# Performance work log

Hardware: AMD Instinct MI355X
Metric: run time of the kernel (lower is better)

## Reference

```python
import jax, jax.numpy as jnp
import numpy as np

HEADS = 16
HEAD_DIM = 64  # embed_size // heads = 1024 // 16


def setup_inputs() -> dict:
    key = jax.random.key(0)
    ks = jax.random.split(key, 9)
    N, Sq, E, C = 4, 2048, 1024, 512
    Skv = 2 * Sq  # keys/values seq must equal doubled query seq (see view trick)
    return {
        "values": jax.random.normal(ks[0], (N, Skv, E), dtype=jnp.float32),
        "keys": jax.random.normal(ks[1], (N, Skv, E), dtype=jnp.float32),
        "queries": jax.random.normal(ks[2], (N, Sq, E), dtype=jnp.float32),
        "mask": jax.random.randint(ks[3], (N, Skv, HEADS, HEADS), 0, 2, dtype=jnp.int32),
        "condition": jax.random.normal(ks[4], (N, Sq, C), dtype=jnp.float32),
        "Wc": jax.random.normal(ks[5], (E, C), dtype=jnp.float32) * 0.02,
        "bc": jax.random.normal(ks[6], (E,), dtype=jnp.float32) * 0.02,
        "Wo": jax.random.normal(ks[7], (E, E), dtype=jnp.float32) * 0.02,
        "bo": jax.random.normal(ks[8], (E,), dtype=jnp.float32) * 0.02,
    }


def reference(values, keys, queries, mask, condition, Wc, bc, Wo, bo):
    N = queries.shape[0]
    H, D = HEADS, HEAD_DIM
    # condition_linear + concat: (N, Sq, 2E) -> view doubles seq -> (N, 2Sq, H, D)
    cond_feat = jnp.einsum('nsc,ec->nse', condition, Wc) + bc
    cq = jnp.concatenate([queries, cond_feat], axis=-1).reshape(N, -1, H, D)
    k = keys.reshape(N, -1, H, D)    # (N, 2Sq, H, D)
    v = values.reshape(N, -1, H, D)  # (N, 2Sq, H, D)
    # per-(batch,seq) heads-by-heads attention, exactly as the torch matmul does
    att = jnp.einsum('nshd,nsed->nshe', cq, k) / jnp.sqrt(jnp.float32(D))
    att = jnp.where(mask == 0, jnp.float32(-1e20), att)
    att = jax.nn.softmax(att, axis=-1)
    out = jnp.einsum('nshe,nsed->nshd', att, v).reshape(N, -1, H * D)
    return jnp.einsum('nsk,ek->nse', out, Wo) + bo
```

## Files before the change

### kernel.cpp

```cpp
#include <hip/hip_runtime.h>
#include <hip/hip_bf16.h>
#include <type_traits>

#define NB   4
#define SQ   2048
#define SKV  4096
#define EMB  1024
#define CDIM 512

typedef __attribute__((ext_vector_type(8))) short short8;
typedef __attribute__((ext_vector_type(4))) float f32x4;

__device__ __forceinline__ float b2f(ushort u) {
    union { unsigned int i; float f; } v;
    v.i = ((unsigned int)u) << 16;
    return v.f;
}
__device__ __forceinline__ ushort f2b(float f) {
    union { float f; unsigned int i; } v; v.f = f;
    unsigned int x = v.i;
    return (ushort)((x + 0x7fffu + ((x >> 16) & 1u)) >> 16);
}

__device__ __forceinline__ void glds16(const ushort* gp, ushort* lp) {
    __builtin_amdgcn_global_load_lds(
        (const __attribute__((address_space(1))) unsigned int*)gp,
        (__attribute__((address_space(3))) unsigned int*)lp,
        16, 0, 0);
}

__global__ __launch_bounds__(256)
void cvt_f32_bf16(const float* __restrict__ in, ushort* __restrict__ out, int n4)
{
    const int i = blockIdx.x * 256 + threadIdx.x;
    if (i < n4) {
        float4 v = ((const float4*)in)[i];
        ushort4 o;
        o.x = f2b(v.x); o.y = f2b(v.y); o.z = f2b(v.z); o.w = f2b(v.w);
        ((ushort4*)out)[i] = o;
    }
}

template <typename OT>
__global__ __launch_bounds__(256)
void gemm_bt_bias(const ushort* __restrict__ A, const ushort* __restrict__ B,
                  const float* __restrict__ bias, OT* __restrict__ C,
                  int M, int Nn, int K)
{
    __shared__ __attribute__((aligned(16))) ushort As[128 * 32];
    __shared__ __attribute__((aligned(16))) ushort Bs[128 * 32];

    const int tid  = threadIdx.x;
    const int wave = tid >> 6;
    const int lane = tid & 63;
    const int quad = lane >> 4;
    const int l16  = lane & 15;
    const int wr   = wave >> 1;
    const int wc   = wave & 1;

    int mTile, nTile;
    {
        const int gx = gridDim.x, gy = gridDim.y;
        const int flat = blockIdx.y * gx + blockIdx.x;
        if ((gx & 7) == 0 && gy == 8) {
            const int c = flat & 7, j = flat >> 3;
            mTile = c * (gx >> 3) + (j >> 3);
            nTile = j & 7;
        } else {
            mTile = blockIdx.x; nTile = blockIdx.y;
        }
    }
    const long mBase = (long)mTile * 128;
    const long nBase = (long)nTile * 128;

    const ushort* Ablk = A + mBase * K;
    const ushort* Bblk = B + nBase * K;

    const int lr = lane >> 2;
    const int lc = (lane & 3) * 8;
    const int c0 = wave * 2, c1 = wave * 2 + 1;
    const ushort* aG0 = Ablk + (long)(c0 * 16 + lr) * K + lc;
    const ushort* aG1 = Ablk + (long)(c1 * 16 + lr) * K + lc;
    const ushort* bG0 = Bblk + (long)(c0 * 16 + lr) * K + lc;
    const ushort* bG1 = Bblk + (long)(c1 * 16 + lr) * K + lc;
    ushort* aL0 = As + c0 * 512;
    ushort* aL1 = As + c1 * 512;
    ushort* bL0 = Bs + c0 * 512;
    ushort* bL1 = Bs + c1 * 512;

    f32x4 acc[4][4];
#pragma unroll
    for (int i = 0; i < 4; ++i)
#pragma unroll
        for (int j = 0; j < 4; ++j)
            acc[i][j] = (f32x4){0.f, 0.f, 0.f, 0.f};

    for (int k0 = 0; k0 < K; k0 += 32) {
        __syncthreads();
        glds16(aG0 + k0, aL0);
        glds16(aG1 + k0, aL1);
        glds16(bG0 + k0, bL0);
        glds16(bG1 + k0, bL1);
        __syncthreads();

        short8 af[4], bfr[4];
#pragma unroll
        for (int mt = 0; mt < 4; ++mt)
            af[mt] = *(const short8*)(As + (wr * 64 + mt * 16 + l16) * 32 + quad * 8);
#pragma unroll
        for (int nt = 0; nt < 4; ++nt)
            bfr[nt] = *(const short8*)(Bs + (wc * 64 + nt * 16 + l16) * 32 + quad * 8);

#pragma unroll
        for (int mt = 0; mt < 4; ++mt)
#pragma unroll
            for (int nt = 0; nt < 4; ++nt)
                acc[mt][nt] = __builtin_amdgcn_mfma_f32_16x16x32_bf16(
                    af[mt], bfr[nt], acc[mt][nt], 0, 0, 0);
    }

#pragma unroll
    for (int mt = 0; mt < 4; ++mt) {
#pragma unroll
        for (int nt = 0; nt < 4; ++nt) {
            const long n = nBase + wc * 64 + nt * 16 + l16;
            const float bv = bias[n];
#pragma unroll
            for (int r = 0; r < 4; ++r) {
                const long m = mBase + wr * 64 + mt * 16 + quad * 4 + r;
                if constexpr (std::is_same<OT, float>::value)
                    C[m * Nn + n] = acc[mt][nt][r] + bv;
                else
                    C[m * Nn + n] = f2b(acc[mt][nt][r] + bv);
            }
        }
    }
}

__global__ __launch_bounds__(256)
void attn_kernel(const float*  __restrict__ queries,
                 const ushort* __restrict__ condfeat,
                 const float*  __restrict__ keys,
                 const float*  __restrict__ values,
                 const int*    __restrict__ mask,
                 ushort* __restrict__ attout)
{
    __shared__ __attribute__((aligned(16))) float vbuf[4][1024];

    const int tid  = threadIdx.x;
    const int wave = tid >> 6;
    const int lane = tid & 63;
    const int l15  = lane & 15;
    const int quad = lane >> 4;
    const int p    = blockIdx.x * 4 + wave;
    const int n    = p >> 12;
    const int sh   = (p & 4095) >> 1;

    float* vb = vbuf[wave];
    const float* vrow = values + ((size_t)p << 10);
#pragma unroll
    for (int c = 0; c < 4; ++c)
        glds16((const ushort*)(vrow + c * 256 + lane * 4),
               (ushort*)(vb + c * 256));

    const int4 mv = *(const int4*)(mask + ((size_t)p << 8) + l15 * 16 + quad * 4);

    union SU { short8 v; ushort u[8]; uint w[4]; };

    const float* krow = keys + ((size_t)p << 10);
    SU ka, kb;
    {
        float kf[16];
        *(float4*)&kf[0]  = *(const float4*)(krow + l15 * 64 + quad * 8);
        *(float4*)&kf[4]  = *(const float4*)(krow + l15 * 64 + quad * 8 + 4);
        *(float4*)&kf[8]  = *(const float4*)(krow + l15 * 64 + 32 + quad * 8);
        *(float4*)&kf[12] = *(const float4*)(krow + l15 * 64 + 32 + quad * 8 + 4);
#pragma unroll
        for (int j = 0; j < 8; ++j) { ka.u[j] = f2b(kf[j]); kb.u[j] = f2b(kf[8 + j]); }
    }

    SU qa, qb;
    if (p & 1) {
        const ushort* crow = condfeat + (((size_t)n * SQ + sh) << 10);
        qa.v = *(const short8*)(crow + l15 * 64 + quad * 8);
        qb.v = *(const short8*)(crow + l15 * 64 + 32 + quad * 8);
    } else {
        const float* qrow = queries + (((size_t)n * SQ + sh) << 10);
        float qf[16];
        *(float4*)&qf[0]  = *(const float4*)(qrow + l15 * 64 + quad * 8);
        *(float4*)&qf[4]  = *(const float4*)(qrow + l15 * 64 + quad * 8 + 4);
        *(float4*)&qf[8]  = *(const float4*)(qrow + l15 * 64 + 32 + quad * 8);
        *(float4*)&qf[12] = *(const float4*)(qrow + l15 * 64 + 32 + quad * 8 + 4);
#pragma unroll
        for (int j = 0; j < 8; ++j) { qa.u[j] = f2b(qf[j]); qb.u[j] = f2b(qf[8 + j]); }
    }

    f32x4 sacc = (f32x4){0.f, 0.f, 0.f, 0.f};
    sacc = __builtin_amdgcn_mfma_f32_16x16x32_bf16(ka.v, qa.v, sacc, 0, 0, 0);
    sacc = __builtin_amdgcn_mfma_f32_16x16x32_bf16(kb.v, qb.v, sacc, 0, 0, 0);

    float s0 = (mv.x == 0) ? -1e20f : sacc[0] * 0.125f;
    float s1 = (mv.y == 0) ? -1e20f : sacc[1] * 0.125f;
    float s2 = (mv.z == 0) ? -1e20f : sacc[2] * 0.125f;
    float s3 = (mv.w == 0) ? -1e20f : sacc[3] * 0.125f;

    float mx = fmaxf(fmaxf(s0, s1), fmaxf(s2, s3));
    mx = fmaxf(mx, __shfl_xor(mx, 16));
    mx = fmaxf(mx, __shfl_xor(mx, 32));
    const float e0 = __expf(s0 - mx), e1 = __expf(s1 - mx);
    const float e2 = __expf(s2 - mx), e3 = __expf(s3 - mx);
    float sum = e0 + e1 + e2 + e3;
    sum += __shfl_xor(sum, 16);
    sum += __shfl_xor(sum, 32);
    const float inv = 1.f / sum;

    const uint pk01 = (uint)f2b(e0 * inv) | ((uint)f2b(e1 * inv) << 16);
    const uint pk23 = (uint)f2b(e2 * inv) | ((uint)f2b(e3 * inv) << 16);

    const int srcA = (quad * 32 + l15) & 63;
    const int srcB = (quad * 32 + 16 + l15) & 63;
    SU pf;
    {
        const uint w0 = (uint)__shfl((int)pk01, srcA);
        const uint w1 = (uint)__shfl((int)pk23, srcA);
        const uint w2 = (uint)__shfl((int)pk01, srcB);
        const uint w3 = (uint)__shfl((int)pk23, srcB);
        const bool lo = (lane < 32);
        pf.w[0] = lo ? w0 : 0u; pf.w[1] = lo ? w1 : 0u;
        pf.w[2] = lo ? w2 : 0u; pf.w[3] = lo ? w3 : 0u;
    }

    asm volatile("s_waitcnt vmcnt(0)" ::: "memory");

    ushort* orow = attout + ((size_t)p << 10);
    const int eb = (quad & 1) * 8;
#pragma unroll
    for (int sl = 0; sl < 4; ++sl) {
        const int d0 = sl * 16;
        SU vf;
#pragma unroll
        for (int j = 0; j < 8; ++j)
            vf.u[j] = f2b(vb[(eb + j) * 64 + d0 + l15]);
        f32x4 oacc = (f32x4){0.f, 0.f, 0.f, 0.f};
        oacc = __builtin_amdgcn_mfma_f32_16x16x32_bf16(vf.v, pf.v, oacc, 0, 0, 0);
        ushort4 o;
        o.x = f2b(oacc[0]); o.y = f2b(oacc[1]);
        o.z = f2b(oacc[2]); o.w = f2b(oacc[3]);
        *(ushort4*)(orow + l15 * 64 + d0 + quad * 4) = o;
    }
}

extern "C" void kernel_launch(void* const* d_in, const int* in_sizes, int n_in,
                              void* d_out, int out_size, void* d_ws, size_t ws_size,
                              hipStream_t stream)
{
    const float* values    = (const float*)d_in[0];
    const float* keys      = (const float*)d_in[1];
    const float* queries   = (const float*)d_in[2];
    const int*   mask      = (const int*)  d_in[3];
    const float* condition = (const float*)d_in[4];
    const float* Wc        = (const float*)d_in[5];
    const float* bc        = (const float*)d_in[6];
    const float* Wo        = (const float*)d_in[7];
    const float* bo        = (const float*)d_in[8];
    float* out = (float*)d_out;

    ushort* condfeat = (ushort*)d_ws;
    ushort* attout   = condfeat + (size_t)NB * SQ * EMB;
    ushort* cond_bf  = attout;
    ushort* Wc_bf    = attout + (size_t)NB * SQ * CDIM;
    ushort* Wo_bf    = condfeat;

    cvt_f32_bf16<<<(NB * SQ * CDIM / 4 + 255) / 256, 256, 0, stream>>>(
        condition, cond_bf, NB * SQ * CDIM / 4);
    cvt_f32_bf16<<<(EMB * CDIM / 4 + 255) / 256, 256, 0, stream>>>(
        Wc, Wc_bf, EMB * CDIM / 4);

    {
        dim3 grid((NB * SQ) / 128, EMB / 128);
        gemm_bt_bias<ushort><<<grid, 256, 0, stream>>>(
            cond_bf, Wc_bf, bc, condfeat, NB * SQ, EMB, CDIM);
    }

    attn_kernel<<<(NB * SKV) / 4, 256, 0, stream>>>(queries, condfeat, keys,
                                                    values, mask, attout);

    cvt_f32_bf16<<<(EMB * EMB / 4 + 255) / 256, 256, 0, stream>>>(
        Wo, Wo_bf, EMB * EMB / 4);

    {
        dim3 grid((NB * SKV) / 128, EMB / 128);
        gemm_bt_bias<float><<<grid, 256, 0, stream>>>(
            attout, Wo_bf, bo, out, NB * SKV, EMB, EMB);
    }
}
```

Measured before the change: 301.6 us.

## Stage K/V/Q through padded bf16 LDS with coalesced block-wide loads

The attention kernel now loads keys, values, queries and condfeat cooperatively across the whole block with contiguous nontemporal vector loads. It converts them to bf16 once and stores them in padded LDS tiles, replacing the strided per-lane global loads and the fp32 LDS buffer for V. Output is staged through LDS so each lane writes 16-byte contiguous stores. This aims to improve coalescing and cut conversion work in a memory-bound kernel, at the cost of a block barrier and extra LDS traffic.

```diff
diff --git a/kernel.cpp b/kernel.cpp
--- a/kernel.cpp
+++ b/kernel.cpp
@@ -7,9 +7,12 @@
 #define SKV  4096
 #define EMB  1024
 #define CDIM 512
+#define POSB 4
 
 typedef __attribute__((ext_vector_type(8))) short short8;
 typedef __attribute__((ext_vector_type(4))) float f32x4;
+typedef __attribute__((ext_vector_type(4))) uint  u32x4;
+typedef __attribute__((ext_vector_type(2))) uint  u32x2;
 
 __device__ __forceinline__ float b2f(ushort u) {
     union { unsigned int i; float f; } v;
@@ -20,6 +23,12 @@
     union { float f; unsigned int i; } v; v.f = f;
     unsigned int x = v.i;
     return (ushort)((x + 0x7fffu + ((x >> 16) & 1u)) >> 16);
+}
+__device__ __forceinline__ u32x2 cvt2(f32x4 v) {
+    u32x2 r;
+    r[0] = (uint)f2b(v[0]) | ((uint)f2b(v[1]) << 16);
+    r[1] = (uint)f2b(v[2]) | ((uint)f2b(v[3]) << 16);
+    return r;
 }
 
 __device__ __forceinline__ void glds16(const ushort* gp, ushort* lp) {
@@ -145,64 +154,78 @@
                  const int*    __restrict__ mask,
                  ushort* __restrict__ attout)
 {
-    __shared__ __attribute__((aligned(16))) float vbuf[4][1024];
+    __shared__ __attribute__((aligned(16))) ushort Kl[POSB * 1088];
+    __shared__ __attribute__((aligned(16))) ushort Vl[POSB * 1088];
+    __shared__ __attribute__((aligned(16))) ushort Ql[POSB * 1088];
 
     const int tid  = threadIdx.x;
     const int wave = tid >> 6;
     const int lane = tid & 63;
     const int l15  = lane & 15;
     const int quad = lane >> 4;
-    const int p    = blockIdx.x * 4 + wave;
-    const int n    = p >> 12;
-    const int sh   = (p & 4095) >> 1;
-
-    float* vb = vbuf[wave];
-    const float* vrow = values + ((size_t)p << 10);
-#pragma unroll
-    for (int c = 0; c < 4; ++c)
-        glds16((const ushort*)(vrow + c * 256 + lane * 4),
-               (ushort*)(vb + c * 256));
-
-    const int4 mv = *(const int4*)(mask + ((size_t)p << 8) + l15 * 16 + quad * 4);
-
-    union SU { short8 v; ushort u[8]; uint w[4]; };
-
-    const float* krow = keys + ((size_t)p << 10);
-    SU ka, kb;
-    {
-        float kf[16];
-        *(float4*)&kf[0]  = *(const float4*)(krow + l15 * 64 + quad * 8);
-        *(float4*)&kf[4]  = *(const float4*)(krow + l15 * 64 + quad * 8 + 4);
-        *(float4*)&kf[8]  = *(const float4*)(krow + l15 * 64 + 32 + quad * 8);
-        *(float4*)&kf[12] = *(const float4*)(krow + l15 * 64 + 32 + quad * 8 + 4);
-#pragma unroll
-        for (int j = 0; j < 8; ++j) { ka.u[j] = f2b(kf[j]); kb.u[j] = f2b(kf[8 + j]); }
-    }
-
-    SU qa, qb;
-    if (p & 1) {
-        const ushort* crow = condfeat + (((size_t)n * SQ + sh) << 10);
-        qa.v = *(const short8*)(crow + l15 * 64 + quad * 8);
-        qb.v = *(const short8*)(crow + l15 * 64 + 32 + quad * 8);
-    } else {
-        const float* qrow = queries + (((size_t)n * SQ + sh) << 10);
-        float qf[16];
-        *(float4*)&qf[0]  = *(const float4*)(qrow + l15 * 64 + quad * 8);
-        *(float4*)&qf[4]  = *(const float4*)(qrow + l15 * 64 + quad * 8 + 4);
-        *(float4*)&qf[8]  = *(const float4*)(qrow + l15 * 64 + 32 + quad * 8);
-        *(float4*)&qf[12] = *(const float4*)(qrow + l15 * 64 + 32 + quad * 8 + 4);
-#pragma unroll
-        for (int j = 0; j < 8; ++j) { qa.u[j] = f2b(qf[j]); qb.u[j] = f2b(qf[8 + j]); }
-    }
+    const int p0   = blockIdx.x * POSB;
+    const int n    = p0 >> 12;
+    const int sh0  = (p0 & 4095) >> 1;
+    const int p    = p0 + wave;
+
+    const f32x4* kg = (const f32x4*)(keys    + ((size_t)p0 << 10)) + tid;
+    const f32x4* vg = (const f32x4*)(values  + ((size_t)p0 << 10)) + tid;
+    const f32x4* qg = (const f32x4*)(queries + (((size_t)n * SQ + sh0) << 10)) + tid;
+    const u32x4* cg = (const u32x4*)(condfeat + (((size_t)n * SQ + sh0) << 10)) + tid;
+
+    f32x4 kv0 = __builtin_nontemporal_load(kg);
+    f32x4 kv1 = __builtin_nontemporal_load(kg + 256);
+    f32x4 kv2 = __builtin_nontemporal_load(kg + 512);
+    f32x4 kv3 = __builtin_nontemporal_load(kg + 768);
+    f32x4 vv0 = __builtin_nontemporal_load(vg);
+    f32x4 vv1 = __builtin_nontemporal_load(vg + 256);
+    f32x4 vv2 = __builtin_nontemporal_load(vg + 512);
+    f32x4 vv3 = __builtin_nontemporal_load(vg + 768);
+    f32x4 qv0 = __builtin_nontemporal_load(qg);
+    f32x4 qv1 = __builtin_nontemporal_load(qg + 256);
+    u32x4 cv  = __builtin_nontemporal_load(cg);
+    u32x4 mv  = __builtin_nontemporal_load(
+        (const u32x4*)(mask + ((size_t)p << 8)) + (l15 * 4 + quad));
+
+    const int eo = (tid >> 4) * 68 + (tid & 15) * 4;
+    *(u32x2*)(Kl + 0 * 1088 + eo) = cvt2(kv0);
+    *(u32x2*)(Kl + 1 * 1088 + eo) = cvt2(kv1);
+    *(u32x2*)(Kl + 2 * 1088 + eo) = cvt2(kv2);
+    *(u32x2*)(Kl + 3 * 1088 + eo) = cvt2(kv3);
+    *(u32x2*)(Vl + 0 * 1088 + eo) = cvt2(vv0);
+    *(u32x2*)(Vl + 1 * 1088 + eo) = cvt2(vv1);
+    *(u32x2*)(Vl + 2 * 1088 + eo) = cvt2(vv2);
+    *(u32x2*)(Vl + 3 * 1088 + eo) = cvt2(vv3);
+    *(u32x2*)(Ql + 0 * 1088 + eo) = cvt2(qv0);
+    *(u32x2*)(Ql + 2 * 1088 + eo) = cvt2(qv1);
+    {
+        const int cp = 1 + ((tid >> 7) << 1);
+        const int co = cp * 1088 + ((tid >> 3) & 15) * 68 + (tid & 7) * 8;
+        *(u32x2*)(Ql + co)     = (u32x2){cv[0], cv[1]};
+        *(u32x2*)(Ql + co + 4) = (u32x2){cv[2], cv[3]};
+    }
+    __syncthreads();
+
+    const ushort* Kw = Kl + wave * 1088;
+    const ushort* Vw = Vl + wave * 1088;
+    ushort*       Qw = Ql + wave * 1088;
+
+    union FU { short8 v; ushort u[8]; uint w[4]; u32x2 q[2]; };
+    const int fo = l15 * 68 + quad * 8;
+    FU ka, kb, qa, qb;
+    ka.q[0] = *(const u32x2*)(Kw + fo);      ka.q[1] = *(const u32x2*)(Kw + fo + 4);
+    kb.q[0] = *(const u32x2*)(Kw + fo + 32); kb.q[1] = *(const u32x2*)(Kw + fo + 36);
+    qa.q[0] = *(const u32x2*)(Qw + fo);      qa.q[1] = *(const u32x2*)(Qw + fo + 4);
+    qb.q[0] = *(const u32x2*)(Qw + fo + 32); qb.q[1] = *(const u32x2*)(Qw + fo + 36);
 
     f32x4 sacc = (f32x4){0.f, 0.f, 0.f, 0.f};
     sacc = __builtin_amdgcn_mfma_f32_16x16x32_bf16(ka.v, qa.v, sacc, 0, 0, 0);
     sacc = __builtin_amdgcn_mfma_f32_16x16x32_bf16(kb.v, qb.v, sacc, 0, 0, 0);
 
-    float s0 = (mv.x == 0) ? -1e20f : sacc[0] * 0.125f;
-    float s1 = (mv.y == 0) ? -1e20f : sacc[1] * 0.125f;
-    float s2 = (mv.z == 0) ? -1e20f : sacc[2] * 0.125f;
-    float s3 = (mv.w == 0) ? -1e20f : sacc[3] * 0.125f;
+    float s0 = (mv[0] == 0u) ? -1e20f : sacc[0] * 0.125f;
+    float s1 = (mv[1] == 0u) ? -1e20f : sacc[1] * 0.125f;
+    float s2 = (mv[2] == 0u) ? -1e20f : sacc[2] * 0.125f;
+    float s3 = (mv[3] == 0u) ? -1e20f : sacc[3] * 0.125f;
 
     float mx = fmaxf(fmaxf(s0, s1), fmaxf(s2, s3));
     mx = fmaxf(mx, __shfl_xor(mx, 16));
@@ -219,7 +242,7 @@
 
     const int srcA = (quad * 32 + l15) & 63;
     const int srcB = (quad * 32 + 16 + l15) & 63;
-    SU pf;
+    FU pf;
     {
         const uint w0 = (uint)__shfl((int)pk01, srcA);
         const uint w1 = (uint)__shfl((int)pk23, srcA);
@@ -230,23 +253,32 @@
         pf.w[2] = lo ? w2 : 0u; pf.w[3] = lo ? w3 : 0u;
     }
 
-    asm volatile("s_waitcnt vmcnt(0)" ::: "memory");
-
-    ushort* orow = attout + ((size_t)p << 10);
     const int eb = (quad & 1) * 8;
 #pragma unroll
     for (int sl = 0; sl < 4; ++sl) {
         const int d0 = sl * 16;
-        SU vf;
+        FU vf;
 #pragma unroll
         for (int j = 0; j < 8; ++j)
-            vf.u[j] = f2b(vb[(eb + j) * 64 + d0 + l15]);
+            vf.u[j] = Vw[(eb + j) * 68 + d0 + l15];
         f32x4 oacc = (f32x4){0.f, 0.f, 0.f, 0.f};
         oacc = __builtin_amdgcn_mfma_f32_16x16x32_bf16(vf.v, pf.v, oacc, 0, 0, 0);
-        ushort4 o;
-        o.x = f2b(oacc[0]); o.y = f2b(oacc[1]);
-        o.z = f2b(oacc[2]); o.w = f2b(oacc[3]);
-        *(ushort4*)(orow + l15 * 64 + d0 + quad * 4) = o;
+        u32x2 ow;
+        ow[0] = (uint)f2b(oacc[0]) | ((uint)f2b(oacc[1]) << 16);
+        ow[1] = (uint)f2b(oacc[2]) | ((uint)f2b(oacc[3]) << 16);
+        *(u32x2*)(Qw + l15 * 68 + d0 + quad * 4) = ow;
+    }
+
+    {
+        const int h1 = lane >> 3, dd = (lane & 7) * 8;
+        FU o1, o2;
+        o1.q[0] = *(const u32x2*)(Qw + h1 * 68 + dd);
+        o1.q[1] = *(const u32x2*)(Qw + h1 * 68 + dd + 4);
+        o2.q[0] = *(const u32x2*)(Qw + (8 + h1) * 68 + dd);
+        o2.q[1] = *(const u32x2*)(Qw + (8 + h1) * 68 + dd + 4);
+        ushort* orow = attout + ((size_t)p << 10);
+        *(short8*)(orow + lane * 8)       = o1.v;
+        *(short8*)(orow + 512 + lane * 8) = o2.v;
     }
 }
 
@@ -282,8 +314,8 @@
             cond_bf, Wc_bf, bc, condfeat, NB * SQ, EMB, CDIM);
     }
 
-    attn_kernel<<<(NB * SKV) / 4, 256, 0, stream>>>(queries, condfeat, keys,
-                                                    values, mask, attout);
+    attn_kernel<<<(NB * SKV) / POSB, 256, 0, stream>>>(queries, condfeat, keys,
+                                                       values, mask, attout);
 
     cvt_f32_bf16<<<(EMB * EMB / 4 + 255) / 256, 256, 0, stream>>>(
         Wo, Wo_bf, EMB * EMB / 4);
```

New measurement: 287.3 us. 1.05x faster.
